# Kernel tuning notes

Hardware: AMD Instinct MI355X
Metric: run time of the kernel (lower is better)

The kernel has to match this reference:

```python
import jax, jax.numpy as jnp
import numpy as np


def _block(x, W, b, use_relu):
    # x: (B, n, dx). Faithful to PairwiseInteractions: full pairwise L2 dist,
    # top-k (k == n) smallest sorted, drop self, concat(self, neighbor), linear,
    # optional relu, mean over the n-1 neighbors.
    B, n, dx = x.shape
    sq = jnp.sum(x * x, axis=-1)                                   # (B, n)
    d2 = sq[:, :, None] + sq[:, None, :] - 2.0 * jnp.einsum('bnd,bmd->bnm', x, x)
    dist = jnp.sqrt(jnp.maximum(d2, 0.0))                          # (B, n, n)
    _, idx = jax.lax.top_k(-dist, n)                               # ascending distances
    idx_nb = idx[:, :, 1:]                                         # drop self -> (B, n, n-1)
    nbr = jnp.take_along_axis(x[:, None, :, :], idx_nb[..., None], axis=2)  # (B, n, n-1, dx)
    self_rep = jnp.broadcast_to(x[:, :, None, :], nbr.shape)
    pairs = jnp.concatenate([self_rep, nbr], axis=-1)              # (B, n, n-1, 2*dx)
    h = pairs @ W + b
    if use_relu:
        h = jax.nn.relu(h)
    return jnp.sum(h, axis=2) / (n - 1)                            # (B, n, d_out)


def setup_inputs() -> dict:
    key = jax.random.key(0)
    ks = jax.random.split(key, 4)
    B, N, d = 2, 1024, 3

    def lin(k, fin, fout):
        kw, kb = jax.random.split(k)
        lim = 1.0 / np.sqrt(fin).astype(np.float32)
        W = jax.random.uniform(kw, (fin, fout), minval=-lim, maxval=lim, dtype=jnp.float32)
        b = jax.random.uniform(kb, (fout,), minval=-lim, maxval=lim, dtype=jnp.float32)
        return W, b

    W1, b1 = lin(ks[1], 2 * d, 32)
    W2, b2 = lin(ks[2], 2 * 32, 64)
    W3, b3 = lin(ks[3], 2 * 64, d)
    x = jax.random.normal(ks[0], (B, N * d), dtype=jnp.float32)
    return {"x": x, "W1": W1, "b1": b1, "W2": W2, "b2": b2, "W3": W3, "b3": b3}


def reference(x, W1, b1, W2, b2, W3, b3):
    B = x.shape[0]
    d = W3.shape[1]
    N = x.shape[1] // d
    h = x.reshape(B, N, d)
    h = _block(h, W1, b1, True)    # eb1: d -> 32, relu
    h = _block(h, W2, b2, True)    # eb2: 32 -> 64, relu
    h = _block(h, W3, b3, False)   # eb3: 64 -> d, no relu
    return h.reshape(B, N * d)
```

## Files before the change

kernel.cpp:

```cpp
#include <hip/hip_runtime.h>

#define NN 1024

__global__ __launch_bounds__(256) void k1_pair32_ac2(
    const float* __restrict__ x,  const float* __restrict__ W1, const float* __restrict__ b1,
    const float* __restrict__ W2, const float* __restrict__ b2,
    float* __restrict__ a2g, float* __restrict__ c2g)
{
    __shared__ float cbuf[8192];
    __shared__ float rowbuf[4][32];

    const int tid  = threadIdx.x;
    const int wave = tid >> 6, lane = tid & 63;
    const int blk  = blockIdx.x;

    const int i  = blk * 4 + wave;
    const int b  = i >> 10;
    const int il = i & 1023;
    const int js = lane >> 5, f = lane & 31;
    const float* xb = x + b * (NN * 3);

    const float xi0 = xb[il*3+0], xi1 = xb[il*3+1], xi2 = xb[il*3+2];
    const float a     = xi0*W1[0*32+f] + xi1*W1[1*32+f] + xi2*W1[2*32+f];
    const float cself = xi0*W1[3*32+f] + xi1*W1[4*32+f] + xi2*W1[5*32+f] + b1[f];

    float acc = 0.f;
    const int f2 = tid & 31, r0 = tid >> 5;
    const float w3f = W1[3*32+f2], w4f = W1[4*32+f2], w5f = W1[5*32+f2], bf = b1[f2];
    for (int tile = 0; tile < NN; tile += 256) {
        #pragma unroll 4
        for (int k = 0; k < 32; ++k) {
            int r = tile + r0 + k*8;
            float y0 = xb[r*3+0], y1 = xb[r*3+1], y2 = xb[r*3+2];
            cbuf[(r0 + k*8)*32 + f2] = y0*w3f + y1*w4f + y2*w5f + bf;
        }
        __syncthreads();
        #pragma unroll 8
        for (int jj = js; jj < 256; jj += 2)
            acc += fmaxf(a + cbuf[jj*32 + f], 0.f);
        __syncthreads();
    }
    acc += __shfl_xor(acc, 32);
    float res = (acc - fmaxf(a + cself, 0.f)) * (1.0f/1023.0f);
    if (js == 0) rowbuf[wave][f] = res;
    __syncthreads();

    float av = 0.f, cv = b2[lane];
    #pragma unroll
    for (int d = 0; d < 32; ++d) {
        float hv = rowbuf[wave][d];
        av += hv * W2[d*64 + lane];
        cv += hv * W2[(32 + d)*64 + lane];
    }
    a2g[i*64 + lane] = av;
    c2g[i*64 + lane] = cv;
}

__global__ __launch_bounds__(256) void k2_pair64_final(
    const float* __restrict__ a2g, const float* __restrict__ c2g,
    const float* __restrict__ W3, const float* __restrict__ b3,
    float* __restrict__ out, float* __restrict__ partials)
{
    __shared__ float cbuf[8192];
    __shared__ float pacc[4][2][64];
    __shared__ float qpart[4][3];

    const int tid  = threadIdx.x;
    const int wave = tid >> 6, lane = tid & 63;
    const int blk  = blockIdx.x;

    const int i0 = blk * 4;
    const int b  = blk >> 8;
    const int rw = wave >> 1, jh = wave & 1;
    const int rowA = i0 + 2*rw, rowB = rowA + 1;

    const float* cb = c2g + b * (NN * 64);
    const float a0 = a2g[rowA*64 + lane];
    const float a1 = a2g[rowB*64 + lane];
    float acc0 = 0.f, acc1 = 0.f;

    for (int tile = 0; tile < NN; tile += 128) {
        const float4* src = (const float4*)(cb + tile * 64);
        float4* dst = (float4*)cbuf;
        for (int k = tid; k < 2048; k += 256) dst[k] = src[k];
        __syncthreads();
        #pragma unroll 8
        for (int k = 0; k < 64; ++k) {
            float c = cbuf[(2*k + jh)*64 + lane];
            acc0 += fmaxf(a0 + c, 0.f);
            acc1 += fmaxf(a1 + c, 0.f);
        }
        __syncthreads();
    }
    pacc[wave][0][lane] = acc0;
    pacc[wave][1][lane] = acc1;
    __syncthreads();

    const int i = i0 + wave;
    const int wpair = 2*(wave >> 1);
    float accf = pacc[wpair][wave & 1][lane] + pacc[wpair + 1][wave & 1][lane];
    float aself = a2g[i*64 + lane];
    float self  = fmaxf(aself + cb[(i & 1023)*64 + lane], 0.f);
    float res = (accf - self) * (1.0f/1023.0f);

    float wt0 = W3[lane*3+0], wt1 = W3[lane*3+1], wt2 = W3[lane*3+2];
    float wb0 = W3[(64+lane)*3+0], wb1 = W3[(64+lane)*3+1], wb2 = W3[(64+lane)*3+2];
    float y0 = res * (wt0 - wb0*(1.0f/1023.0f));
    float y1 = res * (wt1 - wb1*(1.0f/1023.0f));
    float y2 = res * (wt2 - wb2*(1.0f/1023.0f));
    float q0 = res * wb0, q1 = res * wb1, q2 = res * wb2;
    #pragma unroll
    for (int off = 32; off; off >>= 1) {
        y0 += __shfl_xor(y0, off);  y1 += __shfl_xor(y1, off);  y2 += __shfl_xor(y2, off);
        q0 += __shfl_xor(q0, off);  q1 += __shfl_xor(q1, off);  q2 += __shfl_xor(q2, off);
    }
    if (lane == 0) {
        out[i*3+0] = y0 + b3[0];
        out[i*3+1] = y1 + b3[1];
        out[i*3+2] = y2 + b3[2];
        qpart[wave][0] = q0;  qpart[wave][1] = q1;  qpart[wave][2] = q2;
    }
    __syncthreads();
    if (tid < 3)
        partials[blk*3 + tid] = qpart[0][tid] + qpart[1][tid] + qpart[2][tid] + qpart[3][tid];
}

__global__ __launch_bounds__(256) void k3_final(
    const float* __restrict__ partials, float* __restrict__ out)
{
    __shared__ float red[4][3];

    const int tid  = threadIdx.x;
    const int wave = tid >> 6, lane = tid & 63;
    const int blk  = blockIdx.x;
    const int b = blk >> 2;

    const float* pb = partials + b * 256 * 3;
    float s0 = pb[tid*3+0], s1 = pb[tid*3+1], s2 = pb[tid*3+2];
    #pragma unroll
    for (int off = 32; off; off >>= 1) {
        s0 += __shfl_xor(s0, off);  s1 += __shfl_xor(s1, off);  s2 += __shfl_xor(s2, off);
    }
    if (lane == 0) { red[wave][0] = s0; red[wave][1] = s1; red[wave][2] = s2; }
    __syncthreads();
    float S0 = (red[0][0]+red[1][0]+red[2][0]+red[3][0]) * (1.0f/1023.0f);
    float S1 = (red[0][1]+red[1][1]+red[2][1]+red[3][1]) * (1.0f/1023.0f);
    float S2 = (red[0][2]+red[1][2]+red[2][2]+red[3][2]) * (1.0f/1023.0f);

    const int i = b * NN + (blk & 3) * 256 + tid;
    out[i*3+0] += S0;
    out[i*3+1] += S1;
    out[i*3+2] += S2;
}

extern "C" void kernel_launch(void* const* d_in, const int* in_sizes, int n_in,
                              void* d_out, int out_size, void* d_ws, size_t ws_size,
                              hipStream_t stream) {
    const float* x  = (const float*)d_in[0];
    const float* W1 = (const float*)d_in[1];
    const float* b1 = (const float*)d_in[2];
    const float* W2 = (const float*)d_in[3];
    const float* b2 = (const float*)d_in[4];
    const float* W3 = (const float*)d_in[5];
    const float* b3 = (const float*)d_in[6];
    float* out = (float*)d_out;

    float* ws = (float*)d_ws;
    float* a2g      = ws;
    float* c2g      = a2g + 2048*64;
    float* partials = c2g + 2048*64;

    k1_pair32_ac2<<<512, 256, 0, stream>>>(x, W1, b1, W2, b2, a2g, c2g);
    k2_pair64_final<<<512, 256, 0, stream>>>(a2g, c2g, W3, b3, out, partials);
    k3_final<<<8, 256, 0, stream>>>(partials, out);
}
```

Measured before the change: 105.3 us.

## Vectorize pair loops with float2 packed math and reuse LDS tiles across more rows

Both pairwise kernels now use float2 vector arithmetic so the add/max/accumulate can map to packed FP32 instructions. The first kernel stages all of x in shared memory instead of reading it from global memory repeatedly. The second kernel has every wave process all four rows against a shared c tile, which doubles data reuse per LDS load. The cost is more registers, a reworked cross-lane reduction, and a different partial-sum layout, which may affect occupancy.

```diff
diff --git a/kernel.cpp b/kernel.cpp
--- a/kernel.cpp
+++ b/kernel.cpp
@@ -1,4 +1,7 @@
 #include <hip/hip_runtime.h>
+
+typedef float float2v __attribute__((ext_vector_type(2)));
+typedef float float4v __attribute__((ext_vector_type(4)));
 
 #define NN 1024
 
@@ -7,6 +10,7 @@
     const float* __restrict__ W2, const float* __restrict__ b2,
     float* __restrict__ a2g, float* __restrict__ c2g)
 {
+    __shared__ float xbuf[3072];
     __shared__ float cbuf[8192];
     __shared__ float rowbuf[4][32];
 
@@ -17,32 +21,52 @@
     const int i  = blk * 4 + wave;
     const int b  = i >> 10;
     const int il = i & 1023;
-    const int js = lane >> 5, f = lane & 31;
-    const float* xb = x + b * (NN * 3);
-
-    const float xi0 = xb[il*3+0], xi1 = xb[il*3+1], xi2 = xb[il*3+2];
-    const float a     = xi0*W1[0*32+f] + xi1*W1[1*32+f] + xi2*W1[2*32+f];
-    const float cself = xi0*W1[3*32+f] + xi1*W1[4*32+f] + xi2*W1[5*32+f] + b1[f];
-
-    float acc = 0.f;
-    const int f2 = tid & 31, r0 = tid >> 5;
-    const float w3f = W1[3*32+f2], w4f = W1[4*32+f2], w5f = W1[5*32+f2], bf = b1[f2];
+    const int js = lane >> 4;
+    const int fp = lane & 15;
+
+    const float4v* xb4 = (const float4v*)(x + b * 3072);
+    {
+        float4v* xd = (float4v*)xbuf;
+        #pragma unroll
+        for (int n = 0; n < 3; ++n) xd[tid + n * 256] = xb4[tid + n * 256];
+    }
+    __syncthreads();
+
+    const float xi0 = xbuf[il*3+0], xi1 = xbuf[il*3+1], xi2 = xbuf[il*3+2];
+    const float2v* W1v = (const float2v*)W1;
+    const float2v* b1v = (const float2v*)b1;
+    float2v a  = xi0*W1v[0*16+fp] + xi1*W1v[1*16+fp] + xi2*W1v[2*16+fp];
+    float2v cs = xi0*W1v[3*16+fp] + xi1*W1v[4*16+fp] + xi2*W1v[5*16+fp] + b1v[fp];
+
+    const int fp2 = tid & 15, r0 = tid >> 4;
+    const float2v w3 = W1v[3*16+fp2], w4 = W1v[4*16+fp2], w5 = W1v[5*16+fp2];
+    const float2v bb = b1v[fp2];
+
+    float2v acc = (float2v)0.f;
+    float2v* cb2w = (float2v*)cbuf;
+    const float2v* cb2 = (const float2v*)cbuf;
     for (int tile = 0; tile < NN; tile += 256) {
-        #pragma unroll 4
-        for (int k = 0; k < 32; ++k) {
-            int r = tile + r0 + k*8;
-            float y0 = xb[r*3+0], y1 = xb[r*3+1], y2 = xb[r*3+2];
-            cbuf[(r0 + k*8)*32 + f2] = y0*w3f + y1*w4f + y2*w5f + bf;
+        #pragma unroll
+        for (int k = 0; k < 16; ++k) {
+            int r = r0 + k * 16;
+            int g = tile + r;
+            float y0 = xbuf[g*3+0], y1 = xbuf[g*3+1], y2 = xbuf[g*3+2];
+            cb2w[r*16 + fp2] = y0*w3 + y1*w4 + y2*w5 + bb;
         }
         __syncthreads();
         #pragma unroll 8
-        for (int jj = js; jj < 256; jj += 2)
-            acc += fmaxf(a + cbuf[jj*32 + f], 0.f);
-        __syncthreads();
-    }
-    acc += __shfl_xor(acc, 32);
-    float res = (acc - fmaxf(a + cself, 0.f)) * (1.0f/1023.0f);
-    if (js == 0) rowbuf[wave][f] = res;
+        for (int k = 0; k < 64; ++k) {
+            float2v c = cb2[(4*k + js)*16 + fp];
+            acc += __builtin_elementwise_max(a + c, (float2v)0.f);
+        }
+        __syncthreads();
+    }
+    acc.x += __shfl_xor(acc.x, 16);  acc.y += __shfl_xor(acc.y, 16);
+    acc.x += __shfl_xor(acc.x, 32);  acc.y += __shfl_xor(acc.y, 32);
+
+    float2v self = __builtin_elementwise_max(a + cs, (float2v)0.f);
+    float2v res  = (acc - self) * (1.0f/1023.0f);
+    if (js == 0) ((float2v*)rowbuf[wave])[fp] = res;
     __syncthreads();
 
     float av = 0.f, cv = b2[lane];
@@ -62,7 +86,7 @@
     float* __restrict__ out, float* __restrict__ partials)
 {
     __shared__ float cbuf[8192];
-    __shared__ float pacc[4][2][64];
+    __shared__ float2v pacc[4][4][32];
     __shared__ float qpart[4][3];
 
     const int tid  = threadIdx.x;
@@ -71,54 +95,75 @@
 
     const int i0 = blk * 4;
     const int b  = blk >> 8;
-    const int rw = wave >> 1, jh = wave & 1;
-    const int rowA = i0 + 2*rw, rowB = rowA + 1;
+    const int jq = lane >> 5, fp = lane & 31;
 
     const float* cb = c2g + b * (NN * 64);
-    const float a0 = a2g[rowA*64 + lane];
-    const float a1 = a2g[rowB*64 + lane];
-    float acc0 = 0.f, acc1 = 0.f;
-
+    const float2v* a2v = (const float2v*)a2g;
+    const float2v a0 = a2v[(i0+0)*32 + fp];
+    const float2v a1 = a2v[(i0+1)*32 + fp];
+    const float2v a2 = a2v[(i0+2)*32 + fp];
+    const float2v a3 = a2v[(i0+3)*32 + fp];
+    float2v s0 = (float2v)0.f, s1 = (float2v)0.f, s2 = (float2v)0.f, s3 = (float2v)0.f;
+
+    const float4v* src = (const float4v*)cb;
+    const float2v* cb2 = (const float2v*)cbuf;
+    const int jbase = 2*wave + jq;
     for (int tile = 0; tile < NN; tile += 128) {
-        const float4* src = (const float4*)(cb + tile * 64);
-        float4* dst = (float4*)cbuf;
-        for (int k = tid; k < 2048; k += 256) dst[k] = src[k];
-        __syncthreads();
-        #pragma unroll 8
-        for (int k = 0; k < 64; ++k) {
-            float c = cbuf[(2*k + jh)*64 + lane];
-            acc0 += fmaxf(a0 + c, 0.f);
-            acc1 += fmaxf(a1 + c, 0.f);
-        }
-        __syncthreads();
-    }
-    pacc[wave][0][lane] = acc0;
-    pacc[wave][1][lane] = acc1;
+        const float4v* sp = src + tile * 16;
+        float4v* dst = (float4v*)cbuf;
+        #pragma unroll
+        for (int n = 0; n < 8; ++n) dst[tid + n*256] = sp[tid + n*256];
+        __syncthreads();
+        #pragma unroll
+        for (int k = 0; k < 16; ++k) {
+            float2v c = cb2[(8*k + jbase)*32 + fp];
+            s0 += __builtin_elementwise_max(a0 + c, (float2v)0.f);
+            s1 += __builtin_elementwise_max(a1 + c, (float2v)0.f);
+            s2 += __builtin_elementwise_max(a2 + c, (float2v)0.f);
+            s3 += __builtin_elementwise_max(a3 + c, (float2v)0.f);
+        }
+        __syncthreads();
+    }
+    s0.x += __shfl_xor(s0.x, 32);  s0.y += __shfl_xor(s0.y, 32);
+    s1.x += __shfl_xor(s1.x, 32);  s1.y += __shfl_xor(s1.y, 32);
+    s2.x += __shfl_xor(s2.x, 32);  s2.y += __shfl_xor(s2.y, 32);
+    s3.x += __shfl_xor(s3.x, 32);  s3.y += __shfl_xor(s3.y, 32);
+    if (jq == 0) {
+        pacc[wave][0][fp] = s0;  pacc[wave][1][fp] = s1;
+        pacc[wave][2][fp] = s2;  pacc[wave][3][fp] = s3;
+    }
     __syncthreads();
 
     const int i = i0 + wave;
-    const int wpair = 2*(wave >> 1);
-    float accf = pacc[wpair][wave & 1][lane] + pacc[wpair + 1][wave & 1][lane];
-    float aself = a2g[i*64 + lane];
-    float self  = fmaxf(aself + cb[(i & 1023)*64 + lane], 0.f);
-    float res = (accf - self) * (1.0f/1023.0f);
-
-    float wt0 = W3[lane*3+0], wt1 = W3[lane*3+1], wt2 = W3[lane*3+2];
-    float wb0 = W3[(64+lane)*3+0], wb1 = W3[(64+lane)*3+1], wb2 = W3[(64+lane)*3+2];
-    float y0 = res * (wt0 - wb0*(1.0f/1023.0f));
-    float y1 = res * (wt1 - wb1*(1.0f/1023.0f));
-    float y2 = res * (wt2 - wb2*(1.0f/1023.0f));
-    float q0 = res * wb0, q1 = res * wb1, q2 = res * wb2;
-    #pragma unroll
-    for (int off = 32; off; off >>= 1) {
-        y0 += __shfl_xor(y0, off);  y1 += __shfl_xor(y1, off);  y2 += __shfl_xor(y2, off);
-        q0 += __shfl_xor(q0, off);  q1 += __shfl_xor(q1, off);  q2 += __shfl_xor(q2, off);
+    float2v racc = pacc[0][wave][fp] + pacc[1][wave][fp]
+                 + pacc[2][wave][fp] + pacc[3][wave][fp];
+    const float2v* cbv = (const float2v*)cb;
+    const float inv = 1.0f/1023.0f;
+    float2v ai   = a2v[i*32 + fp];
+    float2v self = __builtin_elementwise_max(ai + cbv[(i & 1023)*32 + fp], (float2v)0.f);
+    float2v res  = (racc - self) * inv;
+
+    float y[3], q[3];
+    #pragma unroll
+    for (int t = 0; t < 3; ++t) {
+        float wt0 = W3[(2*fp)*3 + t],   wb0 = W3[(64 + 2*fp)*3 + t];
+        float wt1 = W3[(2*fp+1)*3 + t], wb1 = W3[(64 + 2*fp+1)*3 + t];
+        y[t] = res.x*(wt0 - wb0*inv) + res.y*(wt1 - wb1*inv);
+        q[t] = res.x*wb0 + res.y*wb1;
+    }
+    #pragma unroll
+    for (int off = 1; off < 32; off <<= 1) {
+        #pragma unroll
+        for (int t = 0; t < 3; ++t) {
+            y[t] += __shfl_xor(y[t], off);
+            q[t] += __shfl_xor(q[t], off);
+        }
     }
     if (lane == 0) {
-        out[i*3+0] = y0 + b3[0];
-        out[i*3+1] = y1 + b3[1];
-        out[i*3+2] = y2 + b3[2];
-        qpart[wave][0] = q0;  qpart[wave][1] = q1;  qpart[wave][2] = q2;
+        out[i*3+0] = y[0] + b3[0];
+        out[i*3+1] = y[1] + b3[1];
+        out[i*3+2] = y[2] + b3[2];
+        qpart[wave][0] = q[0];  qpart[wave][1] = q[1];  qpart[wave][2] = q[2];
     }
     __syncthreads();
     if (tid < 3)
@@ -167,8 +212,8 @@
 
     float* ws = (float*)d_ws;
     float* a2g      = ws;
-    float* c2g      = a2g + 2048*64;
-    float* partials = c2g + 2048*64;
+    float* c2g      = a2g + 131072;
+    float* partials = c2g + 131072;
 
     k1_pair32_ac2<<<512, 256, 0, stream>>>(x, W1, b1, W2, b2, a2g, c2g);
     k2_pair64_final<<<512, 256, 0, stream>>>(a2g, c2g, W3, b3, out, partials);
```

Result: no change. 104.5 us, median of 2 (-0.7%).
